# Kernel optimization log

Hardware: AMD Instinct MI355X
Metric: run time of the kernel (lower is better)

The kernel has to match this reference:

```python
import jax, jax.numpy as jnp
import numpy as np

HIDDEN = 160
LN_EPS = 1e-5


def _gru_dir(x_seq, Wih, Whh, bih, bhh, reverse):
    # x_seq: [B,T,D] -> hidden states [B,T,H] (PyTorch GRU gate math)
    B = x_seq.shape[0]
    xW = jnp.einsum('btd,gd->btg', x_seq, Wih) + bih  # [B,T,3H]
    if reverse:
        xW = xW[:, ::-1]

    def step(h, xw):
        g = h @ Whh.T + bhh
        xr, xz, xn = jnp.split(xw, 3, axis=-1)
        hr, hz, hn = jnp.split(g, 3, axis=-1)
        r = jax.nn.sigmoid(xr + hr)
        z = jax.nn.sigmoid(xz + hz)
        n = jnp.tanh(xn + r * hn)
        h_new = (1.0 - z) * n + z * h
        return h_new, h_new

    h0 = jnp.zeros((B, HIDDEN), dtype=x_seq.dtype)
    _, hs = jax.lax.scan(step, h0, jnp.swapaxes(xW, 0, 1))  # [T,B,H]
    hs = jnp.swapaxes(hs, 0, 1)  # [B,T,H]
    if reverse:
        hs = hs[:, ::-1]
    return hs


def _bigru_layer(x_seq, Wih, Whh, bih, bhh):
    f = _gru_dir(x_seq, Wih[0], Whh[0], bih[0], bhh[0], False)
    b = _gru_dir(x_seq, Wih[1], Whh[1], bih[1], bhh[1], True)
    return jnp.concatenate([f, b], axis=-1)  # [B,T,2H]


def setup_inputs() -> dict:
    key = jax.random.key(0)
    ks = jax.random.split(key, 16)
    s = 0.1  # keep activations in a sane range
    d = {
        'x': jax.random.normal(ks[0], (64, 512, 128), jnp.float32),
        'Wih0': s * jax.random.normal(ks[1], (2, 480, 128), jnp.float32),
        'Whh0': s * jax.random.normal(ks[2], (2, 480, 160), jnp.float32),
        'bih0': s * jax.random.normal(ks[3], (2, 480), jnp.float32),
        'bhh0': s * jax.random.normal(ks[4], (2, 480), jnp.float32),
        'Wih1': s * jax.random.normal(ks[5], (2, 480, 320), jnp.float32),
        'Whh1': s * jax.random.normal(ks[6], (2, 480, 160), jnp.float32),
        'bih1': s * jax.random.normal(ks[7], (2, 480), jnp.float32),
        'bhh1': s * jax.random.normal(ks[8], (2, 480), jnp.float32),
        'key_w': s * jax.random.normal(ks[9], (160, 320), jnp.float32),
        'key_b': s * jax.random.normal(ks[10], (160,), jnp.float32),
        'score_w': s * jax.random.normal(ks[11], (4, 160), jnp.float32),
        'score_b': s * jax.random.normal(ks[12], (4,), jnp.float32),
        'proj_w': s * jax.random.normal(ks[13], (256, 320), jnp.float32),
        'proj_b': s * jax.random.normal(ks[14], (256,), jnp.float32),
        'ln_g': jnp.ones((256,), jnp.float32),
        'ln_b': jnp.zeros((256,), jnp.float32),
    }
    return d


def reference(x, Wih0, Whh0, bih0, bhh0, Wih1, Whh1, bih1, bhh1,
              key_w, key_b, score_w, score_b, proj_w, proj_b, ln_g, ln_b):
    # bi-GRU, 2 layers (dropout off in eval)
    h1 = _bigru_layer(x, Wih0, Whh0, bih0, bhh0)   # [B,T,2H]
    seq_out = _bigru_layer(h1, Wih1, Whh1, bih1, bhh1)  # [B,T,2H]

    keys = jnp.tanh(seq_out @ key_w.T + key_b)           # [B,T,H]
    attn_logits = keys @ score_w.T + score_b             # [B,T,heads]

    # motion bias: per-frame displacement norm, z-normalized over time (std is unbiased)
    motion = jnp.linalg.norm(x[:, 1:] - x[:, :-1], axis=-1, keepdims=True)  # [B,T-1,1]
    motion = jnp.concatenate([motion[:, :1], motion], axis=1)               # [B,T,1]
    motion = (motion - motion.mean(axis=1, keepdims=True)) / (
        motion.std(axis=1, keepdims=True, ddof=1) + 1e-6)

    weights = jax.nn.softmax(attn_logits + motion, axis=1)  # [B,T,heads]

    # sum over time of per-head weighted seq_out, then mean over heads
    n_heads = weights.shape[-1]
    pooled = jnp.einsum('btd,bth->bd', seq_out, weights) / n_heads  # [B,2H]

    embedding = pooled @ proj_w.T + proj_b  # dropout=identity in eval
    mu = embedding.mean(axis=-1, keepdims=True)
    var = embedding.var(axis=-1, keepdims=True)
    embedding = (embedding - mu) * jax.lax.rsqrt(var + LN_EPS) * ln_g + ln_b
    embedding = embedding / jnp.maximum(
        jnp.linalg.norm(embedding, axis=-1, keepdims=True), 1e-12)

    return embedding, weights.mean(axis=2)
```

## Files before the change

### kernel.cpp

```cpp
#include <hip/hip_runtime.h>
#include <hip/hip_bf16.h>
#include <math.h>

#define T_SEQ 512
#define BATCH 64
#define DIN   128
#define H     160
#define G3    480

typedef _Float16 half8_t __attribute__((ext_vector_type(8)));
typedef _Float16 half2_t __attribute__((ext_vector_type(2)));

__device__ __forceinline__ float sigmoidf_(float x) {
    return 1.0f / (1.0f + __expf(-x));
}
__device__ __forceinline__ float tanhf_(float x) {
    float a = fabsf(x);
    float e = __expf(2.0f * a);
    float t = 1.0f - 2.0f / (e + 1.0f);
    return copysignf(t, x);
}

__device__ __forceinline__ void dot8(const half8_t h, const half8_t w,
                                     float& a0, float& a1, float& a2, float& a3) {
#if __has_builtin(__builtin_amdgcn_fdot2)
    half2_t h01{h[0], h[1]}, h23{h[2], h[3]}, h45{h[4], h[5]}, h67{h[6], h[7]};
    half2_t w01{w[0], w[1]}, w23{w[2], w[3]}, w45{w[4], w[5]}, w67{w[6], w[7]};
    a0 = __builtin_amdgcn_fdot2(h01, w01, a0, false);
    a1 = __builtin_amdgcn_fdot2(h23, w23, a1, false);
    a2 = __builtin_amdgcn_fdot2(h45, w45, a2, false);
    a3 = __builtin_amdgcn_fdot2(h67, w67, a3, false);
#else
    a0 += (float)h[0] * (float)w[0] + (float)h[1] * (float)w[1];
    a1 += (float)h[2] * (float)w[2] + (float)h[3] * (float)w[3];
    a2 += (float)h[4] * (float)w[4] + (float)h[5] * (float)w[5];
    a3 += (float)h[6] * (float)w[6] + (float)h[7] * (float)w[7];
#endif
}

__device__ __forceinline__ float blockReduceSum(float v, float* red) {
    #pragma unroll
    for (int off = 32; off > 0; off >>= 1) v += __shfl_down(v, off, 64);
    int wave = threadIdx.x >> 6, lane = threadIdx.x & 63;
    __syncthreads();
    if (lane == 0) red[wave] = v;
    __syncthreads();
    float s = red[0];
    int nw = blockDim.x >> 6;
    for (int i = 1; i < nw; ++i) s += red[i];
    return s;
}
__device__ __forceinline__ float blockReduceMax(float v, float* red) {
    #pragma unroll
    for (int off = 32; off > 0; off >>= 1) v = fmaxf(v, __shfl_down(v, off, 64));
    int wave = threadIdx.x >> 6, lane = threadIdx.x & 63;
    __syncthreads();
    if (lane == 0) red[wave] = v;
    __syncthreads();
    float s = red[0];
    int nw = blockDim.x >> 6;
    for (int i = 1; i < nw; ++i) s = fmaxf(s, red[i]);
    return s;
}

__global__ __launch_bounds__(256) void cvt_weights_kernel(
    const float* __restrict__ w0, const float* __restrict__ w1,
    _Float16* __restrict__ out, int n_per)
{
    int i = blockIdx.x * 256 + threadIdx.x;
    if (i < n_per)            out[i] = (_Float16)w0[i];
    else if (i < 2 * n_per)   out[i] = (_Float16)w1[i - n_per];
}

__global__ __launch_bounds__(256) void gemm_bias_kernel(
    const float* __restrict__ A, const float* __restrict__ B,
    const float* __restrict__ bias, float* __restrict__ C,
    int M, int N, int K, int act)
{
    const int BM = 64, BN = 64, BK = 32;
    __shared__ __align__(16) float As[BK][BM];
    __shared__ __align__(16) float Bs[BK][BN];
    int tid  = threadIdx.x;
    int row0 = blockIdx.x * BM;
    int col0 = blockIdx.y * BN;
    int tx = tid & 15, ty = tid >> 4;
    float acc[4][4] = {};

    for (int k0 = 0; k0 < K; k0 += BK) {
        #pragma unroll
        for (int v = 0; v < 2; ++v) {
            int idx = tid + v * 256;
            int m   = idx >> 3;
            int kq  = (idx & 7) << 2;
            float4 a4 = *reinterpret_cast<const float4*>(A + (size_t)(row0 + m) * K + k0 + kq);
            As[kq + 0][m] = a4.x; As[kq + 1][m] = a4.y;
            As[kq + 2][m] = a4.z; As[kq + 3][m] = a4.w;
            float4 b4 = make_float4(0.f, 0.f, 0.f, 0.f);
            if (col0 + m < N)
                b4 = *reinterpret_cast<const float4*>(B + (size_t)(col0 + m) * K + k0 + kq);
            Bs[kq + 0][m] = b4.x; Bs[kq + 1][m] = b4.y;
            Bs[kq + 2][m] = b4.z; Bs[kq + 3][m] = b4.w;
        }
        __syncthreads();
        #pragma unroll
        for (int kk = 0; kk < BK; ++kk) {
            float4 a4 = *reinterpret_cast<const float4*>(&As[kk][ty << 2]);
            float4 b4 = *reinterpret_cast<const float4*>(&Bs[kk][tx << 2]);
            float av[4] = {a4.x, a4.y, a4.z, a4.w};
            float bv[4] = {b4.x, b4.y, b4.z, b4.w};
            #pragma unroll
            for (int i = 0; i < 4; ++i)
                #pragma unroll
                for (int j = 0; j < 4; ++j) acc[i][j] += av[i] * bv[j];
        }
        __syncthreads();
    }
    #pragma unroll
    for (int i = 0; i < 4; ++i) {
        int row = row0 + (ty << 2) + i;
        #pragma unroll
        for (int j = 0; j < 4; ++j) {
            int col = col0 + (tx << 2) + j;
            if (col < N) {
                float v = acc[i][j] + bias[col];
                if (act == 1) v = tanhf_(v);
                C[(size_t)row * N + col] = v;
            }
        }
    }
}

__global__ __launch_bounds__(1024) void gru_kernel(
    const float* __restrict__ xw, const _Float16* __restrict__ whh_h,
    const float* __restrict__ bhh, float* __restrict__ out)
{
    int b    = blockIdx.x >> 1;
    int dir  = blockIdx.x & 1;
    int tid  = threadIdx.x;
    int r    = tid >> 1;
    int half = tid & 1;
    bool active = (tid < 2 * G3);
    __shared__ __align__(16) _Float16 h_h[H];
    __shared__ float g_s[G3];

    half8_t w0 = {}, w1 = {}, w2 = {}, w3 = {}, w4 = {};
    half8_t w5 = {}, w6 = {}, w7 = {}, w8 = {}, w9 = {};
    float bias = 0.f;
    if (active) {
        const half8_t* wp8 = reinterpret_cast<const half8_t*>(
            whh_h + (size_t)dir * G3 * H + (size_t)r * H + half * 80);
        w0 = wp8[0]; w1 = wp8[1]; w2 = wp8[2]; w3 = wp8[3]; w4 = wp8[4];
        w5 = wp8[5]; w6 = wp8[6]; w7 = wp8[7]; w8 = wp8[8]; w9 = wp8[9];
        bias = bhh[dir * G3 + r];
    }
    if (tid < H) h_h[tid] = (_Float16)0.f;
    float hcur = 0.f;
    __syncthreads();

    for (int step = 0; step < T_SEQ; ++step) {
        int tt = dir ? (T_SEQ - 1 - step) : step;
        size_t base = ((size_t)b * T_SEQ + tt) * 960 + (size_t)dir * G3;
        float xr = 0.f, xz = 0.f, xn = 0.f;
        if (tid < H) {
            xr = xw[base + tid];
            xz = xw[base + H + tid];
            xn = xw[base + 2 * H + tid];
        }
        float a0 = 0.f, a1 = 0.f, a2 = 0.f, a3 = 0.f;
        {
            const half8_t* hp8 = reinterpret_cast<const half8_t*>(h_h) + half * 10;
            dot8(hp8[0], w0, a0, a1, a2, a3);
            dot8(hp8[1], w1, a0, a1, a2, a3);
            dot8(hp8[2], w2, a0, a1, a2, a3);
            dot8(hp8[3], w3, a0, a1, a2, a3);
            dot8(hp8[4], w4, a0, a1, a2, a3);
            dot8(hp8[5], w5, a0, a1, a2, a3);
            dot8(hp8[6], w6, a0, a1, a2, a3);
            dot8(hp8[7], w7, a0, a1, a2, a3);
            dot8(hp8[8], w8, a0, a1, a2, a3);
            dot8(hp8[9], w9, a0, a1, a2, a3);
        }
        float s = (a0 + a1) + (a2 + a3);
        s += __shfl_xor(s, 1);
        if (active && half == 0) g_s[r] = s + bias;
        __syncthreads();
        if (tid < H) {
            float rg = sigmoidf_(xr + g_s[tid]);
            float z  = sigmoidf_(xz + g_s[H + tid]);
            float n  = tanhf_(xn + rg * g_s[2 * H + tid]);
            float hn = (1.0f - z) * n + z * hcur;
            hcur = hn;
            h_h[tid] = (_Float16)hn;
            out[((size_t)b * T_SEQ + tt) * 320 + (size_t)dir * H + tid] = hn;
        }
        __syncthreads();
    }
}

__global__ __launch_bounds__(256) void logits_kernel(
    const float* __restrict__ keys, const float* __restrict__ sw,
    const float* __restrict__ sb, float* __restrict__ out)
{
    int gid = blockIdx.x * 256 + threadIdx.x;
    int tok = gid >> 2, h = gid & 3;
    const float4* kr = reinterpret_cast<const float4*>(keys + (size_t)tok * H);
    const float4* wr = reinterpret_cast<const float4*>(sw + (size_t)h * H);
    float acc = 0.f;
    #pragma unroll
    for (int i = 0; i < H / 4; ++i) {
        float4 a = kr[i], w4 = wr[i];
        acc += a.x * w4.x + a.y * w4.y + a.z * w4.z + a.w * w4.w;
    }
    out[gid] = acc + sb[h];
}

__global__ __launch_bounds__(512) void final_kernel(
    const float* __restrict__ x, const float* __restrict__ logits,
    const float* __restrict__ seq, const float* __restrict__ proj_w,
    const float* __restrict__ proj_b, const float* __restrict__ ln_g,
    const float* __restrict__ ln_b, float* __restrict__ out)
{
    int b   = blockIdx.x;
    int tid = threadIdx.x;
    __shared__ float ms[T_SEQ];
    __shared__ float ss[T_SEQ];
    __shared__ __align__(16) float pooled[320];
    __shared__ float red[8];

    {
        float m = 0.f;
        if (tid >= 1) {
            const float4* xc = reinterpret_cast<const float4*>(x + ((size_t)b * T_SEQ + tid) * DIN);
            const float4* xp = reinterpret_cast<const float4*>(x + ((size_t)b * T_SEQ + tid - 1) * DIN);
            float s = 0.f;
            #pragma unroll
            for (int i = 0; i < DIN / 4; ++i) {
                float4 a = xc[i], p = xp[i];
                float dx = a.x - p.x, dy = a.y - p.y, dz = a.z - p.z, dw = a.w - p.w;
                s += dx * dx + dy * dy + dz * dz + dw * dw;
            }
            m = sqrtf(s);
        }
        ms[tid] = m;
    }
    __syncthreads();
    if (tid == 0) ms[0] = ms[1];
    __syncthreads();
    float mv   = ms[tid];
    float mean = blockReduceSum(mv, red) * (1.0f / T_SEQ);
    float var  = blockReduceSum((mv - mean) * (mv - mean), red) * (1.0f / (T_SEQ - 1));
    float mstd = (mv - mean) / (sqrtf(var) + 1e-6f);

    float4 lg = *reinterpret_cast<const float4*>(logits + ((size_t)b * T_SEQ + tid) * 4);
    float l[4] = {lg.x + mstd, lg.y + mstd, lg.z + mstd, lg.w + mstd};
    float ssum = 0.f;
    #pragma unroll
    for (int h = 0; h < 4; ++h) {
        float mx = blockReduceMax(l[h], red);
        float e  = __expf(l[h] - mx);
        float se = blockReduceSum(e, red);
        float wv = e / se;
        ssum += wv;
    }
    float sv = ssum * 0.25f;
    ss[tid] = sv;
    out[16384 + b * T_SEQ + tid] = sv;
    __syncthreads();

    if (tid < 320) {
        float acc = 0.f;
        const float* sp = seq + (size_t)b * T_SEQ * 320 + tid;
        #pragma unroll 4
        for (int t = 0; t < T_SEQ; ++t) acc += sp[(size_t)t * 320] * ss[t];
        pooled[tid] = acc;
    }
    __syncthreads();

    float e = 0.f;
    if (tid < 256) {
        const float4* pw = reinterpret_cast<const float4*>(proj_w + (size_t)tid * 320);
        const float4* pl = reinterpret_cast<const float4*>(pooled);
        float acc = 0.f;
        #pragma unroll
        for (int i = 0; i < 80; ++i) {
            float4 w4 = pw[i], p4 = pl[i];
            acc += w4.x * p4.x + w4.y * p4.y + w4.z * p4.z + w4.w * p4.w;
        }
        e = acc + proj_b[tid];
    }
    float mu = blockReduceSum(tid < 256 ? e : 0.f, red) * (1.0f / 256);
    float dv = (tid < 256) ? (e - mu) : 0.f;
    float vr = blockReduceSum(dv * dv, red) * (1.0f / 256);
    float g  = 0.f;
    if (tid < 256) g = (e - mu) * rsqrtf(vr + 1e-5f) * ln_g[tid] + ln_b[tid];
    float nrm = sqrtf(blockReduceSum(g * g, red));
    nrm = fmaxf(nrm, 1e-12f);
    if (tid < 256) out[b * 256 + tid] = g / nrm;
}

extern "C" void kernel_launch(void* const* d_in, const int* in_sizes, int n_in,
                              void* d_out, int out_size, void* d_ws, size_t ws_size,
                              hipStream_t stream) {
    const float* x       = (const float*)d_in[0];
    const float* Wih0    = (const float*)d_in[1];
    const float* Whh0    = (const float*)d_in[2];
    const float* bih0    = (const float*)d_in[3];
    const float* bhh0    = (const float*)d_in[4];
    const float* Wih1    = (const float*)d_in[5];
    const float* Whh1    = (const float*)d_in[6];
    const float* bih1    = (const float*)d_in[7];
    const float* bhh1    = (const float*)d_in[8];
    const float* key_w   = (const float*)d_in[9];
    const float* key_b   = (const float*)d_in[10];
    const float* score_w = (const float*)d_in[11];
    const float* score_b = (const float*)d_in[12];
    const float* proj_w  = (const float*)d_in[13];
    const float* proj_b  = (const float*)d_in[14];
    const float* ln_g    = (const float*)d_in[15];
    const float* ln_b    = (const float*)d_in[16];

    float* ws    = (float*)d_ws;
    float* xwbuf = ws;
    float* h1    = ws + 31457280;
    float* seq   = h1 + 10485760;
    float* keys  = seq + 10485760;
    float* lgts  = keys + 5242880;
    _Float16* whh_h = (_Float16*)(lgts + 131072);
    float* outf  = (float*)d_out;

    const int M = BATCH * T_SEQ;
    const int NW = 2 * G3 * H;

    cvt_weights_kernel<<<(2 * NW + 255) / 256, 256, 0, stream>>>(Whh0, Whh1, whh_h, NW);
    gemm_bias_kernel<<<dim3(M / 64, 15), 256, 0, stream>>>(x,   Wih0, bih0, xwbuf, M, 960, 128, 0);
    gru_kernel<<<128, 1024, 0, stream>>>(xwbuf, whh_h,        bhh0, h1);
    gemm_bias_kernel<<<dim3(M / 64, 15), 256, 0, stream>>>(h1,  Wih1, bih1, xwbuf, M, 960, 320, 0);
    gru_kernel<<<128, 1024, 0, stream>>>(xwbuf, whh_h + NW,   bhh1, seq);
    gemm_bias_kernel<<<dim3(M / 64, 3),  256, 0, stream>>>(seq, key_w, key_b, keys, M, 160, 320, 1);
    logits_kernel<<<512, 256, 0, stream>>>(keys, score_w, score_b, lgts);
    final_kernel<<<64, 512, 0, stream>>>(x, lgts, seq, proj_w, proj_b, ln_g, ln_b, outf);
}
```

Baseline: 1.436 ms.

## Use fp16 MFMA GEMMs, store GRU outputs in fp16, restructure GRU per-row threads

```diff
diff --git a/kernel.cpp b/kernel.cpp
--- a/kernel.cpp
+++ b/kernel.cpp
@@ -9,7 +9,9 @@
 #define G3    480
 
 typedef _Float16 half8_t __attribute__((ext_vector_type(8)));
+typedef _Float16 half4_t __attribute__((ext_vector_type(4)));
 typedef _Float16 half2_t __attribute__((ext_vector_type(2)));
+typedef float    f32x4   __attribute__((ext_vector_type(4)));
 
 __device__ __forceinline__ float sigmoidf_(float x) {
     return 1.0f / (1.0f + __expf(-x));
@@ -63,126 +65,187 @@
     return s;
 }
 
-__global__ __launch_bounds__(256) void cvt_weights_kernel(
-    const float* __restrict__ w0, const float* __restrict__ w1,
-    _Float16* __restrict__ out, int n_per)
+__global__ __launch_bounds__(256) void cvt_f2h_kernel(
+    const float* __restrict__ src, _Float16* __restrict__ dst, int n4)
 {
     int i = blockIdx.x * 256 + threadIdx.x;
-    if (i < n_per)            out[i] = (_Float16)w0[i];
-    else if (i < 2 * n_per)   out[i] = (_Float16)w1[i - n_per];
-}
-
-__global__ __launch_bounds__(256) void gemm_bias_kernel(
-    const float* __restrict__ A, const float* __restrict__ B,
+    int stride = gridDim.x * 256;
+    for (; i < n4; i += stride) {
+        float4 v = reinterpret_cast<const float4*>(src)[i];
+        half4_t h = {(_Float16)v.x, (_Float16)v.y, (_Float16)v.z, (_Float16)v.w};
+        reinterpret_cast<half4_t*>(dst)[i] = h;
+    }
+}
+
+template<int LDSK>
+__global__ __launch_bounds__(256) void gemm_f16_mfma_kernel(
+    const _Float16* __restrict__ A, const _Float16* __restrict__ B,
     const float* __restrict__ bias, float* __restrict__ C,
-    int M, int N, int K, int act)
+    int N, int K, int act)
 {
-    const int BM = 64, BN = 64, BK = 32;
-    __shared__ __align__(16) float As[BK][BM];
-    __shared__ __align__(16) float Bs[BK][BN];
+    __shared__ _Float16 Bs[64][LDSK];
     int tid  = threadIdx.x;
-    int row0 = blockIdx.x * BM;
-    int col0 = blockIdx.y * BN;
-    int tx = tid & 15, ty = tid >> 4;
-    float acc[4][4] = {};
-
-    for (int k0 = 0; k0 < K; k0 += BK) {
-        #pragma unroll
-        for (int v = 0; v < 2; ++v) {
-            int idx = tid + v * 256;
-            int m   = idx >> 3;
-            int kq  = (idx & 7) << 2;
-            float4 a4 = *reinterpret_cast<const float4*>(A + (size_t)(row0 + m) * K + k0 + kq);
-            As[kq + 0][m] = a4.x; As[kq + 1][m] = a4.y;
-            As[kq + 2][m] = a4.z; As[kq + 3][m] = a4.w;
-            float4 b4 = make_float4(0.f, 0.f, 0.f, 0.f);
-            if (col0 + m < N)
-                b4 = *reinterpret_cast<const float4*>(B + (size_t)(col0 + m) * K + k0 + kq);
-            Bs[kq + 0][m] = b4.x; Bs[kq + 1][m] = b4.y;
-            Bs[kq + 2][m] = b4.z; Bs[kq + 3][m] = b4.w;
-        }
-        __syncthreads();
-        #pragma unroll
-        for (int kk = 0; kk < BK; ++kk) {
-            float4 a4 = *reinterpret_cast<const float4*>(&As[kk][ty << 2]);
-            float4 b4 = *reinterpret_cast<const float4*>(&Bs[kk][tx << 2]);
-            float av[4] = {a4.x, a4.y, a4.z, a4.w};
-            float bv[4] = {b4.x, b4.y, b4.z, b4.w};
+    int lane = tid & 63, wave = tid >> 6;
+    int row0 = blockIdx.x * 64, col0 = blockIdx.y * 64;
+    int kc8 = K >> 3;
+    for (int idx = tid; idx < 64 * kc8; idx += 256) {
+        int rr = idx / kc8, kc = (idx - rr * kc8) << 3;
+        int gcol = col0 + rr;
+        half8_t v = {};
+        if (gcol < N) v = *reinterpret_cast<const half8_t*>(B + (size_t)gcol * K + kc);
+        *reinterpret_cast<half8_t*>(&Bs[rr][kc]) = v;
+    }
+    __syncthreads();
+
+    f32x4 acc0 = {}, acc1 = {}, acc2 = {}, acc3 = {};
+    int arow = row0 + wave * 16 + (lane & 15);
+    int koff = (lane >> 4) << 3;
+    const _Float16* ap = A + (size_t)arow * K + koff;
+    int bl = lane & 15;
+    for (int k0 = 0; k0 < K; k0 += 32) {
+        half8_t a8 = *reinterpret_cast<const half8_t*>(ap + k0);
+        half8_t b0 = *reinterpret_cast<const half8_t*>(&Bs[bl     ][k0 + koff]);
+        half8_t b1 = *reinterpret_cast<const half8_t*>(&Bs[bl + 16][k0 + koff]);
+        half8_t b2 = *reinterpret_cast<const half8_t*>(&Bs[bl + 32][k0 + koff]);
+        half8_t b3 = *reinterpret_cast<const half8_t*>(&Bs[bl + 48][k0 + koff]);
+        acc0 = __builtin_amdgcn_mfma_f32_16x16x32_f16(a8, b0, acc0, 0, 0, 0);
+        acc1 = __builtin_amdgcn_mfma_f32_16x16x32_f16(a8, b1, acc1, 0, 0, 0);
+        acc2 = __builtin_amdgcn_mfma_f32_16x16x32_f16(a8, b2, acc2, 0, 0, 0);
+        acc3 = __builtin_amdgcn_mfma_f32_16x16x32_f16(a8, b3, acc3, 0, 0, 0);
+    }
+
+    int crow = row0 + wave * 16 + ((lane >> 4) << 2);
+    int cb   = col0 + (lane & 15);
+    f32x4 accs[4] = {acc0, acc1, acc2, acc3};
+    #pragma unroll
+    for (int j = 0; j < 4; ++j) {
+        int ccol = cb + j * 16;
+        if (ccol < N) {
+            float bv = bias[ccol];
             #pragma unroll
-            for (int i = 0; i < 4; ++i)
-                #pragma unroll
-                for (int j = 0; j < 4; ++j) acc[i][j] += av[i] * bv[j];
-        }
-        __syncthreads();
-    }
-    #pragma unroll
-    for (int i = 0; i < 4; ++i) {
-        int row = row0 + (ty << 2) + i;
-        #pragma unroll
-        for (int j = 0; j < 4; ++j) {
-            int col = col0 + (tx << 2) + j;
-            if (col < N) {
-                float v = acc[i][j] + bias[col];
-                if (act == 1) v = tanhf_(v);
-                C[(size_t)row * N + col] = v;
+            for (int i = 0; i < 4; ++i) {
+                float v = accs[j][i] + bv;
+                if (act) v = tanhf_(v);
+                C[(size_t)(crow + i) * N + ccol] = v;
             }
         }
     }
 }
 
-__global__ __launch_bounds__(1024) void gru_kernel(
+__global__ __launch_bounds__(512)
+__attribute__((amdgpu_waves_per_eu(2, 2)))
+void gru_kernel(
     const float* __restrict__ xw, const _Float16* __restrict__ whh_h,
-    const float* __restrict__ bhh, float* __restrict__ out)
+    const float* __restrict__ bhh, _Float16* __restrict__ out)
 {
     int b    = blockIdx.x >> 1;
     int dir  = blockIdx.x & 1;
     int tid  = threadIdx.x;
-    int r    = tid >> 1;
-    int half = tid & 1;
-    bool active = (tid < 2 * G3);
+    bool active = (tid < G3);
+    int rc   = active ? tid : 0;
     __shared__ __align__(16) _Float16 h_h[H];
     __shared__ float g_s[G3];
 
-    half8_t w0 = {}, w1 = {}, w2 = {}, w3 = {}, w4 = {};
-    half8_t w5 = {}, w6 = {}, w7 = {}, w8 = {}, w9 = {};
-    float bias = 0.f;
-    if (active) {
-        const half8_t* wp8 = reinterpret_cast<const half8_t*>(
-            whh_h + (size_t)dir * G3 * H + (size_t)r * H + half * 80);
-        w0 = wp8[0]; w1 = wp8[1]; w2 = wp8[2]; w3 = wp8[3]; w4 = wp8[4];
-        w5 = wp8[5]; w6 = wp8[6]; w7 = wp8[7]; w8 = wp8[8]; w9 = wp8[9];
-        bias = bhh[dir * G3 + r];
-    }
+    const _Float16* wp = whh_h + (size_t)dir * G3 * H + (size_t)rc * H;
+    float4 f0, f1, f2, f3, f4, f5, f6, f7, f8, f9;
+    float4 f10, f11, f12, f13, f14, f15, f16, f17, f18, f19;
+    asm volatile("global_load_dwordx4 %0, %1, off"            : "=&v"(f0)  : "v"(wp));
+    asm volatile("global_load_dwordx4 %0, %1, off offset:16"  : "=&v"(f1)  : "v"(wp));
+    asm volatile("global_load_dwordx4 %0, %1, off offset:32"  : "=&v"(f2)  : "v"(wp));
+    asm volatile("global_load_dwordx4 %0, %1, off offset:48"  : "=&v"(f3)  : "v"(wp));
+    asm volatile("global_load_dwordx4 %0, %1, off offset:64"  : "=&v"(f4)  : "v"(wp));
+    asm volatile("global_load_dwordx4 %0, %1, off offset:80"  : "=&v"(f5)  : "v"(wp));
+    asm volatile("global_load_dwordx4 %0, %1, off offset:96"  : "=&v"(f6)  : "v"(wp));
+    asm volatile("global_load_dwordx4 %0, %1, off offset:112" : "=&v"(f7)  : "v"(wp));
+    asm volatile("global_load_dwordx4 %0, %1, off offset:128" : "=&v"(f8)  : "v"(wp));
+    asm volatile("global_load_dwordx4 %0, %1, off offset:144" : "=&v"(f9)  : "v"(wp));
+    asm volatile("global_load_dwordx4 %0, %1, off offset:160" : "=&v"(f10) : "v"(wp));
+    asm volatile("global_load_dwordx4 %0, %1, off offset:176" : "=&v"(f11) : "v"(wp));
+    asm volatile("global_load_dwordx4 %0, %1, off offset:192" : "=&v"(f12) : "v"(wp));
+    asm volatile("global_load_dwordx4 %0, %1, off offset:208" : "=&v"(f13) : "v"(wp));
+    asm volatile("global_load_dwordx4 %0, %1, off offset:224" : "=&v"(f14) : "v"(wp));
+    asm volatile("global_load_dwordx4 %0, %1, off offset:240" : "=&v"(f15) : "v"(wp));
+    asm volatile("global_load_dwordx4 %0, %1, off offset:256" : "=&v"(f16) : "v"(wp));
+    asm volatile("global_load_dwordx4 %0, %1, off offset:272" : "=&v"(f17) : "v"(wp));
+    asm volatile("global_load_dwordx4 %0, %1, off offset:288" : "=&v"(f18) : "v"(wp));
+    asm volatile("global_load_dwordx4 %0, %1, off offset:304" : "=&v"(f19) : "v"(wp));
+    float bias = bhh[dir * G3 + rc];
+    asm volatile("s_waitcnt vmcnt(0)" ::: "memory");
+    __builtin_amdgcn_sched_barrier(0);
+    half8_t w0  = __builtin_bit_cast(half8_t, f0);
+    half8_t w1  = __builtin_bit_cast(half8_t, f1);
+    half8_t w2  = __builtin_bit_cast(half8_t, f2);
+    half8_t w3  = __builtin_bit_cast(half8_t, f3);
+    half8_t w4  = __builtin_bit_cast(half8_t, f4);
+    half8_t w5  = __builtin_bit_cast(half8_t, f5);
+    half8_t w6  = __builtin_bit_cast(half8_t, f6);
+    half8_t w7  = __builtin_bit_cast(half8_t, f7);
+    half8_t w8  = __builtin_bit_cast(half8_t, f8);
+    half8_t w9  = __builtin_bit_cast(half8_t, f9);
+    half8_t w10 = __builtin_bit_cast(half8_t, f10);
+    half8_t w11 = __builtin_bit_cast(half8_t, f11);
+    half8_t w12 = __builtin_bit_cast(half8_t, f12);
+    half8_t w13 = __builtin_bit_cast(half8_t, f13);
+    half8_t w14 = __builtin_bit_cast(half8_t, f14);
+    half8_t w15 = __builtin_bit_cast(half8_t, f15);
+    half8_t w16 = __builtin_bit_cast(half8_t, f16);
+    half8_t w17 = __builtin_bit_cast(half8_t, f17);
+    half8_t w18 = __builtin_bit_cast(half8_t, f18);
+    half8_t w19 = __builtin_bit_cast(half8_t, f19);
+
     if (tid < H) h_h[tid] = (_Float16)0.f;
     float hcur = 0.f;
     __syncthreads();
 
+    float xr = 0.f, xz = 0.f, xn = 0.f;
+    {
+        int tt0 = dir ? (T_SEQ - 1) : 0;
+        size_t base0 = ((size_t)b * T_SEQ + tt0) * 960 + (size_t)dir * G3;
+        if (tid < H) {
+            xr = xw[base0 + tid];
+            xz = xw[base0 + H + tid];
+            xn = xw[base0 + 2 * H + tid];
+        }
+    }
+
     for (int step = 0; step < T_SEQ; ++step) {
         int tt = dir ? (T_SEQ - 1 - step) : step;
-        size_t base = ((size_t)b * T_SEQ + tt) * 960 + (size_t)dir * G3;
-        float xr = 0.f, xz = 0.f, xn = 0.f;
-        if (tid < H) {
-            xr = xw[base + tid];
-            xz = xw[base + H + tid];
-            xn = xw[base + 2 * H + tid];
+        float nxr = 0.f, nxz = 0.f, nxn = 0.f;
+        {
+            int sn  = (step + 1 < T_SEQ) ? step + 1 : step;
+            int ttn = dir ? (T_SEQ - 1 - sn) : sn;
+            size_t basen = ((size_t)b * T_SEQ + ttn) * 960 + (size_t)dir * G3;
+            if (tid < H) {
+                nxr = xw[basen + tid];
+                nxz = xw[basen + H + tid];
+                nxn = xw[basen + 2 * H + tid];
+            }
         }
         float a0 = 0.f, a1 = 0.f, a2 = 0.f, a3 = 0.f;
         {
-            const half8_t* hp8 = reinterpret_cast<const half8_t*>(h_h) + half * 10;
-            dot8(hp8[0], w0, a0, a1, a2, a3);
-            dot8(hp8[1], w1, a0, a1, a2, a3);
-            dot8(hp8[2], w2, a0, a1, a2, a3);
-            dot8(hp8[3], w3, a0, a1, a2, a3);
-            dot8(hp8[4], w4, a0, a1, a2, a3);
-            dot8(hp8[5], w5, a0, a1, a2, a3);
-            dot8(hp8[6], w6, a0, a1, a2, a3);
-            dot8(hp8[7], w7, a0, a1, a2, a3);
-            dot8(hp8[8], w8, a0, a1, a2, a3);
-            dot8(hp8[9], w9, a0, a1, a2, a3);
-        }
-        float s = (a0 + a1) + (a2 + a3);
-        s += __shfl_xor(s, 1);
-        if (active && half == 0) g_s[r] = s + bias;
+            const half8_t* hp8 = reinterpret_cast<const half8_t*>(h_h);
+            dot8(hp8[0],  w0,  a0, a1, a2, a3);
+            dot8(hp8[1],  w1,  a0, a1, a2, a3);
+            dot8(hp8[2],  w2,  a0, a1, a2, a3);
+            dot8(hp8[3],  w3,  a0, a1, a2, a3);
+            dot8(hp8[4],  w4,  a0, a1, a2, a3);
+            dot8(hp8[5],  w5,  a0, a1, a2, a3);
+            dot8(hp8[6],  w6,  a0, a1, a2, a3);
+            dot8(hp8[7],  w7,  a0, a1, a2, a3);
+            dot8(hp8[8],  w8,  a0, a1, a2, a3);
+            dot8(hp8[9],  w9,  a0, a1, a2, a3);
+            dot8(hp8[10], w10, a0, a1, a2, a3);
+            dot8(hp8[11], w11, a0, a1, a2, a3);
+            dot8(hp8[12], w12, a0, a1, a2, a3);
+            dot8(hp8[13], w13, a0, a1, a2, a3);
+            dot8(hp8[14], w14, a0, a1, a2, a3);
+            dot8(hp8[15], w15, a0, a1, a2, a3);
+            dot8(hp8[16], w16, a0, a1, a2, a3);
+            dot8(hp8[17], w17, a0, a1, a2, a3);
+            dot8(hp8[18], w18, a0, a1, a2, a3);
+            dot8(hp8[19], w19, a0, a1, a2, a3);
+        }
+        if (active) g_s[tid] = (a0 + a1) + (a2 + a3) + bias;
         __syncthreads();
         if (tid < H) {
             float rg = sigmoidf_(xr + g_s[tid]);
@@ -191,9 +254,10 @@
             float hn = (1.0f - z) * n + z * hcur;
             hcur = hn;
             h_h[tid] = (_Float16)hn;
-            out[((size_t)b * T_SEQ + tt) * 320 + (size_t)dir * H + tid] = hn;
+            out[((size_t)b * T_SEQ + tt) * 320 + (size_t)dir * H + tid] = (_Float16)hn;
         }
         __syncthreads();
+        xr = nxr; xz = nxz; xn = nxn;
     }
 }
 
@@ -216,7 +280,7 @@
 
 __global__ __launch_bounds__(512) void final_kernel(
     const float* __restrict__ x, const float* __restrict__ logits,
-    const float* __restrict__ seq, const float* __restrict__ proj_w,
+    const _Float16* __restrict__ seq, const float* __restrict__ proj_w,
     const float* __restrict__ proj_b, const float* __restrict__ ln_g,
     const float* __restrict__ ln_b, float* __restrict__ out)
 {
@@ -269,9 +333,9 @@
 
     if (tid < 320) {
         float acc = 0.f;
-        const float* sp = seq + (size_t)b * T_SEQ * 320 + tid;
+        const _Float16* sp = seq + (size_t)b * T_SEQ * 320 + tid;
         #pragma unroll 4
-        for (int t = 0; t < T_SEQ; ++t) acc += sp[(size_t)t * 320] * ss[t];
+        for (int t = 0; t < T_SEQ; ++t) acc += (float)sp[(size_t)t * 320] * ss[t];
         pooled[tid] = acc;
     }
     __syncthreads();
@@ -319,24 +383,37 @@
     const float* ln_g    = (const float*)d_in[15];
     const float* ln_b    = (const float*)d_in[16];
 
+    const int M  = BATCH * T_SEQ;
+    const int NW = 2 * G3 * H;
+
     float* ws    = (float*)d_ws;
     float* xwbuf = ws;
-    float* h1    = ws + 31457280;
-    float* seq   = h1 + 10485760;
-    float* keys  = seq + 10485760;
+    float* keys  = xwbuf + 31457280;
     float* lgts  = keys + 5242880;
-    _Float16* whh_h = (_Float16*)(lgts + 131072);
+    _Float16* h1_h   = (_Float16*)(lgts + 131072);
+    _Float16* seq_h  = h1_h + 10485760;
+    _Float16* x_h    = seq_h + 10485760;
+    _Float16* whh_h  = x_h + 4194304;
+    _Float16* wih0_h = whh_h + 2 * NW;
+    _Float16* wih1_h = wih0_h + 122880;
+    _Float16* keyw_h = wih1_h + 307200;
     float* outf  = (float*)d_out;
 
-    const int M = BATCH * T_SEQ;
-    const int NW = 2 * G3 * H;
-
-    cvt_weights_kernel<<<(2 * NW + 255) / 256, 256, 0, stream>>>(Whh0, Whh1, whh_h, NW);
-    gemm_bias_kernel<<<dim3(M / 64, 15), 256, 0, stream>>>(x,   Wih0, bih0, xwbuf, M, 960, 128, 0);
-    gru_kernel<<<128, 1024, 0, stream>>>(xwbuf, whh_h,        bhh0, h1);
-    gemm_bias_kernel<<<dim3(M / 64, 15), 256, 0, stream>>>(h1,  Wih1, bih1, xwbuf, M, 960, 320, 0);
-    gru_kernel<<<128, 1024, 0, stream>>>(xwbuf, whh_h + NW,   bhh1, seq);
-    gemm_bias_kernel<<<dim3(M / 64, 3),  256, 0, stream>>>(seq, key_w, key_b, keys, M, 160, 320, 1);
+    cvt_f2h_kernel<<<150, 256, 0, stream>>>(Whh0, whh_h, NW / 4);
+    cvt_f2h_kernel<<<150, 256, 0, stream>>>(Whh1, whh_h + NW, NW / 4);
+    cvt_f2h_kernel<<<120, 256, 0, stream>>>(Wih0, wih0_h, 122880 / 4);
+    cvt_f2h_kernel<<<300, 256, 0, stream>>>(Wih1, wih1_h, 307200 / 4);
+    cvt_f2h_kernel<<<50,  256, 0, stream>>>(key_w, keyw_h, 51200 / 4);
+    cvt_f2h_kernel<<<2048, 256, 0, stream>>>(x, x_h, 4194304 / 4);
+
+    gemm_f16_mfma_kernel<144><<<dim3(M / 64, 15), 256, 0, stream>>>(
+        x_h, wih0_h, bih0, xwbuf, 960, 128, 0);
+    gru_kernel<<<128, 512, 0, stream>>>(xwbuf, whh_h, bhh0, h1_h);
+    gemm_f16_mfma_kernel<336><<<dim3(M / 64, 15), 256, 0, stream>>>(
+        h1_h, wih1_h, bih1, xwbuf, 960, 320, 0);
+    gru_kernel<<<128, 512, 0, stream>>>(xwbuf, whh_h + NW, bhh1, seq_h);
+    gemm_f16_mfma_kernel<336><<<dim3(M / 64, 3), 256, 0, stream>>>(
+        seq_h, keyw_h, key_b, keys, 160, 320, 1);
     logits_kernel<<<512, 256, 0, stream>>>(keys, score_w, score_b, lgts);
-    final_kernel<<<64, 512, 0, stream>>>(x, lgts, seq, proj_w, proj_b, ln_g, ln_b, outf);
-}
+    final_kernel<<<64, 512, 0, stream>>>(x, lgts, seq_h, proj_w, proj_b, ln_g, ln_b, outf);
+}
```

New measurement: 1.206 ms. 16.0% less time.
